# Optimization experiments

Measured on AMD Instinct MI355X. Metric: run time of the kernel, lower is better.

## Reference

```python
import jax, jax.numpy as jnp
import numpy as np

D = 1024      # d_model
H = 16        # num_heads
DK = D // H   # head dim
L = 6         # num_layers
DFF = 4 * D   # feed-forward width
V = 32000     # vocab
B = 8         # batch
TP1 = 513     # target tokens (x length); decoded length = 512
S = 1024      # encoder frames
MAXLEN = 512
EPS = 1e-6


def make_pe(max_len, d):
    pos = np.arange(max_len, dtype=np.float64)[:, None]
    i = np.arange(0, d, 2, dtype=np.float64)[None, :]
    ang = pos / np.power(10000.0, i / d)
    pe = np.zeros((max_len, d), dtype=np.float32)
    pe[:, 0::2] = np.sin(ang)
    pe[:, 1::2] = np.cos(ang)
    return jnp.asarray(pe)


def setup_inputs() -> dict:
    key = jax.random.key(0)
    ks = jax.random.split(key, 16)
    sc = 0.02
    inp = {
        'x': jax.random.randint(ks[0], (B, TP1), 0, V, dtype=jnp.int64),
        'encoder_output': jax.random.normal(ks[1], (B, S, D), jnp.float32),
        'emb': jax.random.normal(ks[2], (V, D), jnp.float32) * sc,
        'pe': make_pe(MAXLEN, D),
        # per-layer stacked params; index 0..3 = q,k,v,out projections (in,out layout)
        'attn1_w': jax.random.normal(ks[3], (L, 4, D, D), jnp.float32) * sc,
        'attn1_b': jnp.zeros((L, 4, D), jnp.float32),
        'attn2_w': jax.random.normal(ks[4], (L, 4, D, D), jnp.float32) * sc,
        'attn2_b': jnp.zeros((L, 4, D), jnp.float32),
        'norm_a': jnp.ones((L, 3, D), jnp.float32),
        'norm_b': jnp.zeros((L, 3, D), jnp.float32),
        'ff1_w': jax.random.normal(ks[5], (L, D, DFF), jnp.float32) * sc,
        'ff1_b': jnp.zeros((L, DFF), jnp.float32),
        'ff2_w': jax.random.normal(ks[6], (L, DFF, D), jnp.float32) * sc,
        'ff2_b': jnp.zeros((L, D), jnp.float32),
        'fc_w': jax.random.normal(ks[7], (D, V), jnp.float32) * sc,
        'fc_b': jnp.zeros((V,), jnp.float32),
    }
    return inp


def _norm(x, a, b):
    mu = jnp.mean(x, axis=-1, keepdims=True)
    # torch .std() default is unbiased (ddof=1)
    var = jnp.sum((x - mu) ** 2, axis=-1, keepdims=True) / (x.shape[-1] - 1)
    return a * (x - mu) / (jnp.sqrt(var) + EPS) + b


def _mha(q_in, kv_in, w, b):
    # w: [4, D, D], b: [4, D]; masks in the original are no-ops (bug), omitted.
    bs, tq, _ = q_in.shape
    q = (q_in @ w[0] + b[0]).reshape(bs, tq, H, DK).transpose(0, 2, 1, 3)
    k = (kv_in @ w[1] + b[1]).reshape(bs, -1, H, DK).transpose(0, 2, 1, 3)
    v = (kv_in @ w[2] + b[2]).reshape(bs, -1, H, DK).transpose(0, 2, 1, 3)
    score = jnp.einsum('bhqd,bhkd->bhqk', q, k) / np.sqrt(DK).astype(np.float32)
    attn = jax.nn.softmax(score, axis=-1)
    o = jnp.einsum('bhqk,bhkd->bhqd', attn, v)
    o = o.transpose(0, 2, 1, 3).reshape(bs, tq, D)
    return o @ w[3] + b[3]


def reference(x, encoder_output, emb, pe, attn1_w, attn1_b, attn2_w, attn2_b,
              norm_a, norm_b, ff1_w, ff1_b, ff2_w, ff2_b, fc_w, fc_b):
    t = x.shape[1] - 1
    h = emb[x[:, :-1]] + pe[None, :t, :]  # [B, T, D]
    for l in range(L):
        a1 = _mha(h, h, attn1_w[l], attn1_b[l])
        h = _norm(a1 + h, norm_a[l, 0], norm_b[l, 0])
        a2 = _mha(h, encoder_output, attn2_w[l], attn2_b[l])
        h = _norm(a2 + h, norm_a[l, 1], norm_b[l, 1])
        f = jax.nn.relu(h @ ff1_w[l] + ff1_b[l]) @ ff2_w[l] + ff2_b[l]
        h = _norm(f + h, norm_a[l, 2], norm_b[l, 2])
    logits = h @ fc_w + fc_b  # [B, T, V]
    return jax.nn.log_softmax(logits, axis=-1)
```

## Files before the change

kernel.cpp:

```cpp
#include <hip/hip_runtime.h>

typedef __attribute__((ext_vector_type(4))) float f32x4;
typedef __attribute__((ext_vector_type(8))) __bf16 bfx8;
typedef unsigned short u16;
typedef unsigned int u32;

__device__ __forceinline__ u16 f2bf(float f) {
  u32 u = __builtin_bit_cast(u32, f);
  u = (u + 0x7FFFu + ((u >> 16) & 1u)) >> 16;
  return (u16)u;
}
__device__ __forceinline__ float bf2f(u16 u) {
  return __builtin_bit_cast(float, ((u32)u) << 16);
}

typedef __attribute__((address_space(1))) const void gvoid;
typedef __attribute__((address_space(3))) void svoid;
__device__ __forceinline__ void gload16(const void* g, void* l) {
  __builtin_amdgcn_global_load_lds((gvoid*)g, (svoid*)l, 16, 0, 0);
}

__device__ __forceinline__ float wredsum(float v) {
#pragma unroll
  for (int o = 32; o; o >>= 1) v += __shfl_xor(v, o, 64);
  return v;
}
__device__ __forceinline__ float wredmax(float v) {
#pragma unroll
  for (int o = 32; o; o >>= 1) v = fmaxf(v, __shfl_xor(v, o, 64));
  return v;
}

__global__ __launch_bounds__(256) void wconv_kernel(const float* __restrict__ in,
                                                    u16* __restrict__ out, int K, int N) {
  __shared__ u16 tile[32][33];
  const long z = blockIdx.z;
  const float* iz = in + z * (long)K * N;
  u16* oz = out + z * (long)K * N;
  const int n0 = blockIdx.x << 5, k0 = blockIdx.y << 5;
  const int tx = threadIdx.x & 31, ty = threadIdx.x >> 5;
#pragma unroll
  for (int i = 0; i < 4; ++i)
    tile[ty + 8 * i][tx] = f2bf(iz[(long)(k0 + ty + 8 * i) * N + n0 + tx]);
  __syncthreads();
#pragma unroll
  for (int i = 0; i < 4; ++i)
    oz[(long)(n0 + ty + 8 * i) * K + k0 + tx] = tile[tx][ty + 8 * i];
}

__global__ __launch_bounds__(256) void cvt_kernel(const float* __restrict__ in,
                                                  u16* __restrict__ out, long n) {
  long i = ((long)blockIdx.x * 256 + threadIdx.x) * 4;
  if (i + 3 < n) {
    float4 v = *(const float4*)(in + i);
    ushort4 o = {f2bf(v.x), f2bf(v.y), f2bf(v.z), f2bf(v.w)};
    *(ushort4*)(out + i) = o;
  }
}

__global__ __launch_bounds__(256) void embed_kernel(const int* __restrict__ x,
                                                    const float* __restrict__ emb,
                                                    const float* __restrict__ pe,
                                                    float* __restrict__ h,
                                                    u16* __restrict__ hb) {
  const int row = blockIdx.x;
  const int b = row >> 9, t = row & 511;
  const long tok = (long)x[b * 513 + t];
  const int d = threadIdx.x << 2;
  float4 e = *(const float4*)(emb + tok * 1024 + d);
  float4 p = *(const float4*)(pe + (long)t * 1024 + d);
  float4 v = {e.x + p.x, e.y + p.y, e.z + p.z, e.w + p.w};
  *(float4*)(h + (long)row * 1024 + d) = v;
  ushort4 o = {f2bf(v.x), f2bf(v.y), f2bf(v.z), f2bf(v.w)};
  *(ushort4*)(hb + (long)row * 1024 + d) = o;
}

__global__ __launch_bounds__(256) void addnorm_kernel(const float* __restrict__ delta,
                                                      float* __restrict__ h,
                                                      u16* __restrict__ hb,
                                                      const float* __restrict__ ga,
                                                      const float* __restrict__ gb) {
  __shared__ float r1[4], r2[4];
  const long row = blockIdx.x;
  const int d = threadIdx.x << 2;
  float4 a = *(const float4*)(h + row * 1024 + d);
  float4 q = *(const float4*)(delta + row * 1024 + d);
  float x0 = a.x + q.x, x1 = a.y + q.y, x2 = a.z + q.z, x3 = a.w + q.w;
  float s1 = wredsum(x0 + x1 + x2 + x3);
  float s2 = wredsum(x0 * x0 + x1 * x1 + x2 * x2 + x3 * x3);
  if ((threadIdx.x & 63) == 0) { r1[threadIdx.x >> 6] = s1; r2[threadIdx.x >> 6] = s2; }
  __syncthreads();
  float S1 = r1[0] + r1[1] + r1[2] + r1[3];
  float S2 = r2[0] + r2[1] + r2[2] + r2[3];
  float mu = S1 * (1.0f / 1024.0f);
  float var = (S2 - S1 * mu) * (1.0f / 1023.0f);
  float inv = 1.0f / (sqrtf(fmaxf(var, 0.f)) + 1e-6f);
  float4 g4 = *(const float4*)(ga + d);
  float4 b4 = *(const float4*)(gb + d);
  float y0 = g4.x * (x0 - mu) * inv + b4.x;
  float y1 = g4.y * (x1 - mu) * inv + b4.y;
  float y2 = g4.z * (x2 - mu) * inv + b4.z;
  float y3 = g4.w * (x3 - mu) * inv + b4.w;
  float4 y = {y0, y1, y2, y3};
  *(float4*)(h + row * 1024 + d) = y;
  ushort4 o = {f2bf(y0), f2bf(y1), f2bf(y2), f2bf(y3)};
  *(ushort4*)(hb + row * 1024 + d) = o;
}

__global__ __launch_bounds__(256) void logsoftmax_kernel(float* __restrict__ lg) {
  const long row = blockIdx.x;
  float* lr = lg + row * 32000L;
  float m = -1e30f, s = 0.f;
  for (int j = threadIdx.x; j < 8000; j += 256) {
    float4 v = *(const float4*)(lr + (long)j * 4);
    float lm = fmaxf(fmaxf(v.x, v.y), fmaxf(v.z, v.w));
    if (lm > m) { s *= __expf(m - lm); m = lm; }
    s += __expf(v.x - m) + __expf(v.y - m) + __expf(v.z - m) + __expf(v.w - m);
  }
#pragma unroll
  for (int o = 32; o; o >>= 1) {
    float om = __shfl_xor(m, o, 64), os = __shfl_xor(s, o, 64);
    float M = fmaxf(m, om);
    s = s * __expf(m - M) + os * __expf(om - M);
    m = M;
  }
  __shared__ float rm[4], rs[4];
  if ((threadIdx.x & 63) == 0) { rm[threadIdx.x >> 6] = m; rs[threadIdx.x >> 6] = s; }
  __syncthreads();
  float M = fmaxf(fmaxf(rm[0], rm[1]), fmaxf(rm[2], rm[3]));
  float S = rs[0] * __expf(rm[0] - M) + rs[1] * __expf(rm[1] - M) +
            rs[2] * __expf(rm[2] - M) + rs[3] * __expf(rm[3] - M);
  float lse = M + __logf(S);
  for (int j = threadIdx.x; j < 8000; j += 256) {
    float4 v = *(const float4*)(lr + (long)j * 4);
    v.x -= lse; v.y -= lse; v.z -= lse; v.w -= lse;
    *(float4*)(lr + (long)j * 4) = v;
  }
}

__global__ __launch_bounds__(512) void logsoftmax_bf16_kernel(const u16* __restrict__ lg,
                                                              float* __restrict__ out) {
  __shared__ float rr[8];
  const long row = blockIdx.x;
  const u16* lr = lg + row * 32000L;
  float* od = out + row * 32000L;
  const int tid = threadIdx.x;
  float m0 = -1e30f, m1 = -1e30f;
  for (int j = tid * 8; j < 32000; j += 4096) {
    ushort4 a = *(const ushort4*)(lr + j);
    ushort4 b = *(const ushort4*)(lr + j + 4);
    m0 = fmaxf(m0, fmaxf(fmaxf(bf2f(a.x), bf2f(a.y)), fmaxf(bf2f(a.z), bf2f(a.w))));
    m1 = fmaxf(m1, fmaxf(fmaxf(bf2f(b.x), bf2f(b.y)), fmaxf(bf2f(b.z), bf2f(b.w))));
  }
  float m = wredmax(fmaxf(m0, m1));
  if ((tid & 63) == 0) rr[tid >> 6] = m;
  __syncthreads();
  m = fmaxf(fmaxf(fmaxf(rr[0], rr[1]), fmaxf(rr[2], rr[3])),
            fmaxf(fmaxf(rr[4], rr[5]), fmaxf(rr[6], rr[7])));
  __syncthreads();
  float s0 = 0.f, s1 = 0.f;
  for (int j = tid * 8; j < 32000; j += 4096) {
    ushort4 a = *(const ushort4*)(lr + j);
    ushort4 b = *(const ushort4*)(lr + j + 4);
    s0 += __expf(bf2f(a.x) - m) + __expf(bf2f(a.y) - m) +
          __expf(bf2f(a.z) - m) + __expf(bf2f(a.w) - m);
    s1 += __expf(bf2f(b.x) - m) + __expf(bf2f(b.y) - m) +
          __expf(bf2f(b.z) - m) + __expf(bf2f(b.w) - m);
  }
  float s = wredsum(s0 + s1);
  if ((tid & 63) == 0) rr[tid >> 6] = s;
  __syncthreads();
  s = rr[0] + rr[1] + rr[2] + rr[3] + rr[4] + rr[5] + rr[6] + rr[7];
  const float lse = m + __logf(s);
  for (int j = tid * 8; j < 32000; j += 4096) {
    ushort4 a = *(const ushort4*)(lr + j);
    ushort4 b = *(const ushort4*)(lr + j + 4);
    float4 o0 = {bf2f(a.x) - lse, bf2f(a.y) - lse, bf2f(a.z) - lse, bf2f(a.w) - lse};
    float4 o1 = {bf2f(b.x) - lse, bf2f(b.y) - lse, bf2f(b.z) - lse, bf2f(b.w) - lse};
    *(float4*)(od + j) = o0;
    *(float4*)(od + j + 4) = o1;
  }
}

template <int SKV>
__global__ __launch_bounds__(256) void attn_kernel(const u16* __restrict__ Q,
                                                   const u16* __restrict__ Kb,
                                                   const u16* __restrict__ Vt,
                                                   u16* __restrict__ ctx) {
  __shared__ u16 Kl[4096];
  __shared__ u16 Vl[4096];
  __shared__ u16 Pl[4][16][72];
  const int tid = threadIdx.x, lane = tid & 63, wave = tid >> 6;
  const int l15 = lane & 15, lg = lane >> 4;
  const int bh = blockIdx.y;
  const int qrow = blockIdx.x * 64 + wave * 16 + l15;
  const u16* qp = Q + ((long)bh * 512 + qrow) * 64 + lg * 8;
  bfx8 qf0 = *(const bfx8*)(qp);
  bfx8 qf1 = *(const bfx8*)(qp + 32);

  const int srow = tid >> 3;
  const int schunk = (tid & 7) ^ (srow & 7);
  const u16* Kbb = Kb + ((long)bh * SKV + srow) * 64 + schunk * 8;
  const u16* Vtb2 = Vt + ((long)bh * 64 + srow) * SKV + schunk * 8;

  const f32x4 zf = {0.f, 0.f, 0.f, 0.f};
  f32x4 acc_o[4] = {zf, zf, zf, zf};
  float mrun = -1e30f, lrun = 0.f;
  const int swk = l15 & 7;

#pragma unroll 1
  for (int kv0 = 0; kv0 < SKV; kv0 += 64) {
    gload16(Kbb + (long)kv0 * 64, &Kl[tid * 8]);
    gload16(Kbb + (long)(kv0 + 32) * 64, &Kl[2048 + tid * 8]);
    gload16(Vtb2 + kv0, &Vl[tid * 8]);
    gload16(Vtb2 + (long)32 * SKV + kv0, &Vl[2048 + tid * 8]);
    __syncthreads();
    f32x4 sacc[4];
#pragma unroll
    for (int kvt = 0; kvt < 4; ++kvt) {
      const int krow = kvt * 16 + l15;
      bfx8 kf0 = *(const bfx8*)&Kl[krow * 64 + ((lg ^ swk) << 3)];
      bfx8 kf1 = *(const bfx8*)&Kl[krow * 64 + (((4 + lg) ^ swk) << 3)];
      f32x4 t = __builtin_amdgcn_mfma_f32_16x16x32_bf16(kf0, qf0, zf, 0, 0, 0);
      sacc[kvt] = __builtin_amdgcn_mfma_f32_16x16x32_bf16(kf1, qf1, t, 0, 0, 0);
    }
    float pm = -1e30f;
#pragma unroll
    for (int kvt = 0; kvt < 4; ++kvt)
#pragma unroll
      for (int r = 0; r < 4; ++r) pm = fmaxf(pm, sacc[kvt][r]);
    pm = fmaxf(pm, __shfl_xor(pm, 16, 64));
    pm = fmaxf(pm, __shfl_xor(pm, 32, 64));
    pm *= 0.125f;
    const float mnew = fmaxf(mrun, pm);
    const float corr = __expf(mrun - mnew);
    float psum = 0.f;
#pragma unroll
    for (int kvt = 0; kvt < 4; ++kvt)
#pragma unroll
      for (int r = 0; r < 4; ++r) {
        float p = __expf(sacc[kvt][r] * 0.125f - mnew);
        psum += p;
        Pl[wave][l15][kvt * 16 + lg * 4 + r] = f2bf(p);
      }
    psum += __shfl_xor(psum, 16, 64);
    psum += __shfl_xor(psum, 32, 64);
    lrun = lrun * corr + psum;
    mrun = mnew;
#pragma unroll
    for (int dt = 0; dt < 4; ++dt) {
      acc_o[dt][0] *= corr; acc_o[dt][1] *= corr;
      acc_o[dt][2] *= corr; acc_o[dt][3] *= corr;
    }
    bfx8 pf0 = *(const bfx8*)&Pl[wave][l15][lg * 8];
    bfx8 pf1 = *(const bfx8*)&Pl[wave][l15][32 + lg * 8];
#pragma unroll
    for (int dt = 0; dt < 4; ++dt) {
      const int vrow = dt * 16 + l15;
      bfx8 vf0 = *(const bfx8*)&Vl[vrow * 64 + ((lg ^ swk) << 3)];
      bfx8 vf1 = *(const bfx8*)&Vl[vrow * 64 + (((4 + lg) ^ swk) << 3)];
      acc_o[dt] = __builtin_amdgcn_mfma_f32_16x16x32_bf16(vf0, pf0, acc_o[dt], 0, 0, 0);
      acc_o[dt] = __builtin_amdgcn_mfma_f32_16x16x32_bf16(vf1, pf1, acc_o[dt], 0, 0, 0);
    }
    __syncthreads();
  }
  const float inv = 1.0f / lrun;
  const int b = bh >> 4, hh = bh & 15;
  u16* crow = ctx + ((long)b * 512 + qrow) * 1024 + hh * 64;
#pragma unroll
  for (int dt = 0; dt < 4; ++dt)
#pragma unroll
    for (int r = 0; r < 4; ++r)
      crow[dt * 16 + lg * 4 + r] = f2bf(acc_o[dt][r] * inv);
}

template <int BM, int BN, int WMW, int WNW, int EPI, bool RELU>
__global__ __launch_bounds__(256) void gemm_bt(const u16* __restrict__ A, long sAz, int lda,
                                               const u16* __restrict__ Bt, long sBz, int ldb,
                                               const float* __restrict__ bias,
                                               void* __restrict__ out, long sCz, int ldc,
                                               int K, int Ttok) {
  constexpr int WROWS = BM / WMW, WCOLS = BN / WNW;
  constexpr int MI = WROWS / 16, NI = WCOLS / 16;
  __shared__ u16 As[BM * 32];
  __shared__ u16 Bs[BN * 32];
  const int tid = threadIdx.x, lane = tid & 63, wave = tid >> 6;
  const int l15 = lane & 15, lg = lane >> 4;
  const int wm = wave / WNW, wn = wave % WNW;
  const int bx = blockIdx.x, by = blockIdx.y;
  const long z = blockIdx.z;
  const int srow = tid >> 2, scol = (tid & 3) << 3;
  const u16* Aa = A + z * sAz + (long)(by * BM + srow) * lda + scol;
  const u16* Ba = Bt + z * sBz + (long)(bx * BN + srow) * ldb + scol;

  f32x4 acc[MI][NI];
#pragma unroll
  for (int i = 0; i < MI; ++i)
#pragma unroll
    for (int j = 0; j < NI; ++j) acc[i][j] = (f32x4){0.f, 0.f, 0.f, 0.f};

  for (int kt = 0; kt < K; kt += 32) {
#pragma unroll
    for (int i = 0; i < BM / 64; ++i)
      gload16(Aa + (long)i * 64 * lda + kt, &As[i * 2048 + tid * 8]);
#pragma unroll
    for (int i = 0; i < BN / 64; ++i)
      gload16(Ba + (long)i * 64 * ldb + kt, &Bs[i * 2048 + tid * 8]);
    __syncthreads();
    bfx8 afr[MI], bfr[NI];
#pragma unroll
    for (int i = 0; i < MI; ++i)
      afr[i] = *(const bfx8*)&As[(wm * WROWS + i * 16 + l15) * 32 + (lg << 3)];
#pragma unroll
    for (int j = 0; j < NI; ++j)
      bfr[j] = *(const bfx8*)&Bs[(wn * WCOLS + j * 16 + l15) * 32 + (lg << 3)];
#pragma unroll
    for (int i = 0; i < MI; ++i)
#pragma unroll
      for (int j = 0; j < NI; ++j)
        acc[i][j] = __builtin_amdgcn_mfma_f32_16x16x32_bf16(afr[i], bfr[j], acc[i][j], 0, 0, 0);
    __syncthreads();
  }

  const int gm0 = by * BM + wm * WROWS;
  const int gn0 = bx * BN + wn * WCOLS;
#pragma unroll
  for (int i = 0; i < MI; ++i) {
#pragma unroll
    for (int j = 0; j < NI; ++j) {
      const int gn = gn0 + j * 16 + l15;
      const float bv = bias ? bias[gn] : 0.f;
#pragma unroll
      for (int r = 0; r < 4; ++r) {
        const int gm = gm0 + i * 16 + (lg << 2) + r;
        float v = acc[i][j][r] + bv;
        if (RELU) v = fmaxf(v, 0.f);
        if constexpr (EPI == 0) {
          ((float*)out)[z * sCz + (long)gm * ldc + gn] = v;
        } else if constexpr (EPI == 1) {
          ((u16*)out)[z * sCz + (long)gm * ldc + gn] = f2bf(v);
        } else if constexpr (EPI == 3) {
          const int b = gm / Ttok, t = gm - b * Ttok;
          const int hh = gn >> 6, dk = gn & 63;
          ((u16*)out)[(((long)(b * 16 + hh) * Ttok + t) << 6) + dk] = f2bf(v);
        }
      }
    }
  }
}

#define MMAQ(hm, hn)                                                                   \
  {                                                                                    \
    _Pragma("unroll") for (int kk = 0; kk < 2; ++kk)                                   \
        _Pragma("unroll") for (int i = 0; i < 4; ++i)                                  \
            _Pragma("unroll") for (int jn = 0; jn < 2; ++jn)                           \
                acc[(hm)*4 + i][(hn)*2 + jn] = __builtin_amdgcn_mfma_f32_16x16x32_bf16( \
                    a[i][kk], b[jn][kk], acc[(hm)*4 + i][(hn)*2 + jn], 0, 0, 0);       \
  }

template <int EPI, bool RELU>
__global__ __launch_bounds__(512, 2) void gemm256(const u16* __restrict__ A, int lda,
                                                  const u16* __restrict__ Bt, int ldb,
                                                  const float* __restrict__ bias,
                                                  void* __restrict__ out, int ldc, int K,
                                                  int Ttok, void* __restrict__ out2,
                                                  void* __restrict__ out3, int gx) {
  __shared__ u16 lds[2][2][2][8192];
  const int tid = threadIdx.x, lane = tid & 63;
  const int wid = tid >> 6, wm = wid >> 2, wn = wid & 3;
  const int l15 = lane & 15, lg = lane >> 4;
  const int nwg = gridDim.x;
  int wg = blockIdx.x;
  wg = (wg & 7) * (nwg >> 3) + (wg >> 3);
  const int mt = wg % gx, nt_ = wg / gx;
  const int NT = K >> 6;

  const int r0 = tid >> 3;
  const int blkx = (tid & 7) ^ (r0 & 7);
  const u16* Abase = A + (long)(mt * 256 + r0) * lda + blkx * 8;
  const u16* Bbase = Bt + (long)(nt_ * 256 + r0) * ldb + blkx * 8;

  auto stageA = [&](int s, int half) {
    const int kts = (s < NT ? s : NT - 1) << 6;
    const u16* g = Abase + (long)(half * 128) * lda + kts;
    gload16(g, &lds[s & 1][0][half][tid * 8]);
    gload16(g + (long)64 * lda, &lds[s & 1][0][half][(512 + tid) * 8]);
  };
  auto stageB = [&](int s, int half) {
    const int kts = (s < NT ? s : NT - 1) << 6;
    const u16* g = Bbase + (long)(half * 128) * ldb + kts;
    gload16(g, &lds[s & 1][1][half][tid * 8]);
    gload16(g + (long)64 * ldb, &lds[s & 1][1][half][(512 + tid) * 8]);
  };

  f32x4 acc[8][4];
#pragma unroll
  for (int i = 0; i < 8; ++i)
#pragma unroll
    for (int j = 0; j < 4; ++j) acc[i][j] = (f32x4){0.f, 0.f, 0.f, 0.f};
  bfx8 a[4][2], b[2][2];

  const int sw = l15 & 7;
  auto loadA = [&](int buf, int hm) {
#pragma unroll
    for (int i = 0; i < 4; ++i) {
      const int row = hm * 64 + i * 16 + l15;
#pragma unroll
      for (int kk = 0; kk < 2; ++kk)
        a[i][kk] = *(const bfx8*)&lds[buf][0][wm][row * 64 + (((kk * 4 + lg) ^ sw) << 3)];
    }
  };
  auto loadB = [&](int buf, int hn) {
#pragma unroll
    for (int jn = 0; jn < 2; ++jn) {
      const int row = (wn & 1) * 64 + hn * 32 + jn * 16 + l15;
#pragma unroll
      for (int kk = 0; kk < 2; ++kk)
        b[jn][kk] = *(const bfx8*)&lds[buf][1][wn >> 1][row * 64 + (((kk * 4 + lg) ^ sw) << 3)];
    }
  };

  stageA(0, 0); stageA(0, 1); stageB(0, 0); stageB(0, 1);
  stageA(1, 0); stageA(1, 1);
  asm volatile("s_waitcnt vmcnt(4)" ::: "memory");
  __builtin_amdgcn_s_barrier();

  for (int t = 0; t < NT; ++t) {
    const int p = t & 1;
    loadA(p, 0); loadB(p, 0);
    stageB(t + 1, 0);
    __builtin_amdgcn_s_barrier();
    asm volatile("s_waitcnt lgkmcnt(0)" ::: "memory");
    __builtin_amdgcn_s_setprio(1);
    MMAQ(0, 0);
    __builtin_amdgcn_s_setprio(0);
    __builtin_amdgcn_s_barrier();
    loadB(p, 1);
    stageB(t + 1, 1);
    __builtin_amdgcn_s_barrier();
    asm volatile("s_waitcnt lgkmcnt(0)" ::: "memory");
    __builtin_amdgcn_s_setprio(1);
    MMAQ(0, 1);
    __builtin_amdgcn_s_setprio(0);
    __builtin_amdgcn_s_barrier();
    loadA(p, 1); loadB(p, 0);
    stageA(t + 2, 0);
    __builtin_amdgcn_s_barrier();
    asm volatile("s_waitcnt lgkmcnt(0)" ::: "memory");
    __builtin_amdgcn_s_setprio(1);
    MMAQ(1, 0);
    __builtin_amdgcn_s_setprio(0);
    __builtin_amdgcn_s_barrier();
    loadB(p, 1);
    stageA(t + 2, 1);
    asm volatile("s_waitcnt vmcnt(4)" ::: "memory");
    __builtin_amdgcn_s_barrier();
    asm volatile("s_waitcnt lgkmcnt(0)" ::: "memory");
    __builtin_amdgcn_s_setprio(1);
    MMAQ(1, 1);
    __builtin_amdgcn_s_setprio(0);
    __builtin_amdgcn_s_barrier();
  }

  const int gm0 = mt * 256 + wm * 128;
  const int gn0 = nt_ * 256 + wn * 64;
#pragma unroll
  for (int ii = 0; ii < 8; ++ii) {
#pragma unroll
    for (int jj = 0; jj < 4; ++jj) {
      const int gn = gn0 + jj * 16 + l15;
      const float bv = bias ? bias[gn] : 0.f;
#pragma unroll
      for (int r = 0; r < 4; ++r) {
        const int gm = gm0 + ii * 16 + (lg << 2) + r;
        float v = acc[ii][jj][r] + bv;
        if (RELU) v = fmaxf(v, 0.f);
        if constexpr (EPI == 0) {
          ((float*)out)[(long)gm * ldc + gn] = v;
        } else if constexpr (EPI == 1) {
          ((u16*)out)[(long)gm * ldc + gn] = f2bf(v);
        } else if constexpr (EPI == 6) {
          const int bq = gm / Ttok, t2 = gm - bq * Ttok;
          const int sec = gn >> 10, w1 = gn & 1023;
          const int hh = w1 >> 6, dk = w1 & 63;
          const u16 val = f2bf(v);
          if (sec == 0)
            ((u16*)out)[(((long)(bq * 16 + hh) * Ttok + t2) << 6) + dk] = val;
          else if (sec == 1)
            ((u16*)out2)[(((long)(bq * 16 + hh) * Ttok + t2) << 6) + dk] = val;
          else
            ((u16*)out3)[((long)((bq * 16 + hh) << 6) + dk) * Ttok + t2] = val;
        } else if constexpr (EPI == 7) {
          const int bq = gm / Ttok, t2 = gm - bq * Ttok;
          const int sec = gn >> 10, w1 = gn & 1023;
          const int hh = w1 >> 6, dk = w1 & 63;
          const u16 val = f2bf(v);
          if (sec == 0)
            ((u16*)out)[(((long)(bq * 16 + hh) * Ttok + t2) << 6) + dk] = val;
          else
            ((u16*)out2)[((long)((bq * 16 + hh) << 6) + dk) * Ttok + t2] = val;
        }
      }
    }
  }
}

extern "C" void kernel_launch(void* const* d_in, const int* in_sizes, int n_in,
                              void* d_out, int out_size, void* d_ws, size_t ws_size,
                              hipStream_t stream) {
  const int* x = (const int*)d_in[0];
  const float* enc = (const float*)d_in[1];
  const float* emb = (const float*)d_in[2];
  const float* pe = (const float*)d_in[3];
  const float* a1w = (const float*)d_in[4];
  const float* a1b = (const float*)d_in[5];
  const float* a2w = (const float*)d_in[6];
  const float* a2b = (const float*)d_in[7];
  const float* nra = (const float*)d_in[8];
  const float* nrb = (const float*)d_in[9];
  const float* f1w = (const float*)d_in[10];
  const float* f1b = (const float*)d_in[11];
  const float* f2w = (const float*)d_in[12];
  const float* f2b = (const float*)d_in[13];
  const float* fcw = (const float*)d_in[14];
  const float* fcb = (const float*)d_in[15];
  float* out = (float*)d_out;

  char* base = (char*)d_ws;
  size_t off = 0;
  auto alloc = [&](size_t bytes) -> void* {
    void* p = base + off;
    off += (bytes + 255) & ~(size_t)255;
    return p;
  };
  const long wsz = 1024 * 1024;
  const bool big = ws_size >= (600ull << 20);
  u16* wT = (u16*)alloc(96ull * wsz * 2);
  u16* encb = (u16*)alloc(8ull * wsz * 2);
  float* h = (float*)alloc(4ull * wsz * 4);
  u16* hb = (u16*)alloc(4ull * wsz * 2);
  u16* qb = (u16*)alloc(4ull * wsz * 2);
  u16* kb = (u16*)alloc(8ull * wsz * 2);
  u16* vtb = (u16*)alloc(8ull * wsz * 2);
  u16* ctxb = (u16*)alloc(4ull * wsz * 2);
  float* af = (float*)alloc(4ull * wsz * 4);
  u16* midb = (u16*)alloc(16ull * wsz * 2);
  u16* fcT = qb;
  u16* lgb = big ? (u16*)alloc(4096ull * 32000 * 2) : nullptr;

  u16* wTa1 = wT;
  u16* wTa2 = wT + 24 * wsz;
  u16* wTf1 = wT + 48 * wsz;
  u16* wTf2 = wT + 72 * wsz;

  cvt_kernel<<<dim3(8192), dim3(256), 0, stream>>>(enc, encb, 8ll * wsz);
  embed_kernel<<<dim3(4096), dim3(256), 0, stream>>>(x, emb, pe, h, hb);
  wconv_kernel<<<dim3(32, 32, 24), dim3(256), 0, stream>>>(a1w, wTa1, 1024, 1024);
  wconv_kernel<<<dim3(32, 32, 24), dim3(256), 0, stream>>>(a2w, wTa2, 1024, 1024);
  wconv_kernel<<<dim3(128, 32, 6), dim3(256), 0, stream>>>(f1w, wTf1, 1024, 4096);
  wconv_kernel<<<dim3(32, 128, 6), dim3(256), 0, stream>>>(f2w, wTf2, 4096, 1024);

  for (int l = 0; l < 6; ++l) {
    const float* b1 = a1b + (long)l * 4096;
    const float* b2 = a2b + (long)l * 4096;
    const u16* w1 = wTa1 + (long)l * 4 * wsz;
    const u16* w2 = wTa2 + (long)l * 4 * wsz;

    gemm256<6, false><<<dim3(192), dim3(512), 0, stream>>>(
        hb, 1024, w1, 1024, b1, qb, 0, 1024, 512, kb, vtb, 16);
    attn_kernel<512><<<dim3(8, 128), dim3(256), 0, stream>>>(qb, kb, vtb, ctxb);
    gemm_bt<128, 128, 2, 2, 0, false><<<dim3(8, 32, 1), dim3(256), 0, stream>>>(
        ctxb, 0, 1024, w1 + 3 * wsz, 0, 1024, b1 + 3072, af, 0, 1024, 1024, 0);
    addnorm_kernel<<<dim3(4096), dim3(256), 0, stream>>>(af, h, hb, nra + (l * 3 + 0) * 1024,
                                                         nrb + (l * 3 + 0) * 1024);

    gemm_bt<128, 128, 2, 2, 3, false><<<dim3(8, 32, 1), dim3(256), 0, stream>>>(
        hb, 0, 1024, w2, 0, 1024, b2, qb, 0, 0, 1024, 512);
    gemm256<7, false><<<dim3(256), dim3(512), 0, stream>>>(
        encb, 1024, w2 + wsz, 1024, b2 + 1024, kb, 0, 1024, 1024, vtb, nullptr, 32);
    attn_kernel<1024><<<dim3(8, 128), dim3(256), 0, stream>>>(qb, kb, vtb, ctxb);
    gemm_bt<128, 128, 2, 2, 0, false><<<dim3(8, 32, 1), dim3(256), 0, stream>>>(
        ctxb, 0, 1024, w2 + 3 * wsz, 0, 1024, b2 + 3072, af, 0, 1024, 1024, 0);
    addnorm_kernel<<<dim3(4096), dim3(256), 0, stream>>>(af, h, hb, nra + (l * 3 + 1) * 1024,
                                                         nrb + (l * 3 + 1) * 1024);

    gemm256<1, true><<<dim3(256), dim3(512), 0, stream>>>(
        hb, 1024, wTf1 + (long)l * 4 * wsz, 1024, f1b + (long)l * 4096, midb, 4096, 1024, 0,
        nullptr, nullptr, 16);
    gemm_bt<128, 128, 2, 2, 0, false><<<dim3(8, 32, 1), dim3(256), 0, stream>>>(
        midb, 0, 4096, wTf2 + (long)l * 4 * wsz, 0, 4096, f2b + (long)l * 1024, af, 0, 1024,
        4096, 0);
    addnorm_kernel<<<dim3(4096), dim3(256), 0, stream>>>(af, h, hb, nra + (l * 3 + 2) * 1024,
                                                         nrb + (l * 3 + 2) * 1024);
  }

  wconv_kernel<<<dim3(1000, 32, 1), dim3(256), 0, stream>>>(fcw, fcT, 1024, 32000);
  if (big) {
    gemm256<1, false><<<dim3(2000), dim3(512), 0, stream>>>(
        hb, 1024, fcT, 1024, fcb, lgb, 32000, 1024, 0, nullptr, nullptr, 16);
    logsoftmax_bf16_kernel<<<dim3(4096), dim3(512), 0, stream>>>(lgb, out);
  } else {
    gemm256<0, false><<<dim3(2000), dim3(512), 0, stream>>>(
        hb, 1024, fcT, 1024, fcb, out, 32000, 1024, 0, nullptr, nullptr, 16);
    logsoftmax_kernel<<<dim3(4096), dim3(256), 0, stream>>>(out);
  }
}
```

Baseline: 3.652 ms.

## Split-K the N=1024 GEMMs, sum partials in addnorm, cache logits rows in LDS

The output-projection and FF2 GEMMs now run 2-way split-K (grid z=2). Each split writes a separate fp32 partial, bias is applied only on z=0, and addnorm sums both partials with the residual. This doubles the block count from 256 to 512 so more work is in flight, at the cost of one extra fp32 partial buffer written and read per addnorm. The bf16 log-softmax stages each 32000-element row into 64KB of LDS, so the max, sum and output passes read global logits once instead of three times, which may lower occupancy. The gemm256 block-to-tile mapping is also changed for XCD locality.

```diff
diff --git a/kernel.cpp b/kernel.cpp
--- a/kernel.cpp
+++ b/kernel.cpp
@@ -76,6 +76,7 @@
 }
 
 __global__ __launch_bounds__(256) void addnorm_kernel(const float* __restrict__ delta,
+                                                      const float* __restrict__ delta2,
                                                       float* __restrict__ h,
                                                       u16* __restrict__ hb,
                                                       const float* __restrict__ ga,
@@ -85,7 +86,9 @@
   const int d = threadIdx.x << 2;
   float4 a = *(const float4*)(h + row * 1024 + d);
   float4 q = *(const float4*)(delta + row * 1024 + d);
-  float x0 = a.x + q.x, x1 = a.y + q.y, x2 = a.z + q.z, x3 = a.w + q.w;
+  float4 q2 = *(const float4*)(delta2 + row * 1024 + d);
+  float x0 = a.x + q.x + q2.x, x1 = a.y + q.y + q2.y;
+  float x2 = a.z + q.z + q2.z, x3 = a.w + q.w + q2.w;
   float s1 = wredsum(x0 + x1 + x2 + x3);
   float s2 = wredsum(x0 * x0 + x1 * x1 + x2 * x2 + x3 * x3);
   if ((threadIdx.x & 63) == 0) { r1[threadIdx.x >> 6] = s1; r2[threadIdx.x >> 6] = s2; }
@@ -140,6 +143,7 @@
 
 __global__ __launch_bounds__(512) void logsoftmax_bf16_kernel(const u16* __restrict__ lg,
                                                               float* __restrict__ out) {
+  __shared__ u16 rl[32000];
   __shared__ float rr[8];
   const long row = blockIdx.x;
   const u16* lr = lg + row * 32000L;
@@ -149,6 +153,8 @@
   for (int j = tid * 8; j < 32000; j += 4096) {
     ushort4 a = *(const ushort4*)(lr + j);
     ushort4 b = *(const ushort4*)(lr + j + 4);
+    *(ushort4*)&rl[j] = a;
+    *(ushort4*)&rl[j + 4] = b;
     m0 = fmaxf(m0, fmaxf(fmaxf(bf2f(a.x), bf2f(a.y)), fmaxf(bf2f(a.z), bf2f(a.w))));
     m1 = fmaxf(m1, fmaxf(fmaxf(bf2f(b.x), bf2f(b.y)), fmaxf(bf2f(b.z), bf2f(b.w))));
   }
@@ -160,8 +166,8 @@
   __syncthreads();
   float s0 = 0.f, s1 = 0.f;
   for (int j = tid * 8; j < 32000; j += 4096) {
-    ushort4 a = *(const ushort4*)(lr + j);
-    ushort4 b = *(const ushort4*)(lr + j + 4);
+    ushort4 a = *(const ushort4*)&rl[j];
+    ushort4 b = *(const ushort4*)&rl[j + 4];
     s0 += __expf(bf2f(a.x) - m) + __expf(bf2f(a.y) - m) +
           __expf(bf2f(a.z) - m) + __expf(bf2f(a.w) - m);
     s1 += __expf(bf2f(b.x) - m) + __expf(bf2f(b.y) - m) +
@@ -173,8 +179,8 @@
   s = rr[0] + rr[1] + rr[2] + rr[3] + rr[4] + rr[5] + rr[6] + rr[7];
   const float lse = m + __logf(s);
   for (int j = tid * 8; j < 32000; j += 4096) {
-    ushort4 a = *(const ushort4*)(lr + j);
-    ushort4 b = *(const ushort4*)(lr + j + 4);
+    ushort4 a = *(const ushort4*)&rl[j];
+    ushort4 b = *(const ushort4*)&rl[j + 4];
     float4 o0 = {bf2f(a.x) - lse, bf2f(a.y) - lse, bf2f(a.z) - lse, bf2f(a.w) - lse};
     float4 o1 = {bf2f(b.x) - lse, bf2f(b.y) - lse, bf2f(b.z) - lse, bf2f(b.w) - lse};
     *(float4*)(od + j) = o0;
@@ -329,7 +335,7 @@
 #pragma unroll
     for (int j = 0; j < NI; ++j) {
       const int gn = gn0 + j * 16 + l15;
-      const float bv = bias ? bias[gn] : 0.f;
+      const float bv = (bias && z == 0) ? bias[gn] : 0.f;
 #pragma unroll
       for (int r = 0; r < 4; ++r) {
         const int gm = gm0 + i * 16 + (lg << 2) + r;
@@ -369,10 +375,10 @@
   const int tid = threadIdx.x, lane = tid & 63;
   const int wid = tid >> 6, wm = wid >> 2, wn = wid & 3;
   const int l15 = lane & 15, lg = lane >> 4;
-  const int nwg = gridDim.x;
-  int wg = blockIdx.x;
-  wg = (wg & 7) * (nwg >> 3) + (wg >> 3);
-  const int mt = wg % gx, nt_ = wg / gx;
+  const int S = gx >> 3;
+  const int xcd = blockIdx.x & 7, idx = blockIdx.x >> 3;
+  const int mt = xcd * S + idx % S;
+  const int nt_ = idx / S;
   const int NT = K >> 6;
 
   const int r0 = tid >> 3;
@@ -544,6 +550,7 @@
   u16* vtb = (u16*)alloc(8ull * wsz * 2);
   u16* ctxb = (u16*)alloc(4ull * wsz * 2);
   float* af = (float*)alloc(4ull * wsz * 4);
+  float* af2 = (float*)alloc(4ull * wsz * 4);
   u16* midb = (u16*)alloc(16ull * wsz * 2);
   u16* fcT = qb;
   u16* lgb = big ? (u16*)alloc(4096ull * 32000 * 2) : nullptr;
@@ -569,29 +576,29 @@
     gemm256<6, false><<<dim3(192), dim3(512), 0, stream>>>(
         hb, 1024, w1, 1024, b1, qb, 0, 1024, 512, kb, vtb, 16);
     attn_kernel<512><<<dim3(8, 128), dim3(256), 0, stream>>>(qb, kb, vtb, ctxb);
-    gemm_bt<128, 128, 2, 2, 0, false><<<dim3(8, 32, 1), dim3(256), 0, stream>>>(
-        ctxb, 0, 1024, w1 + 3 * wsz, 0, 1024, b1 + 3072, af, 0, 1024, 1024, 0);
-    addnorm_kernel<<<dim3(4096), dim3(256), 0, stream>>>(af, h, hb, nra + (l * 3 + 0) * 1024,
-                                                         nrb + (l * 3 + 0) * 1024);
+    gemm_bt<128, 128, 2, 2, 0, false><<<dim3(8, 32, 2), dim3(256), 0, stream>>>(
+        ctxb, 512, 1024, w1 + 3 * wsz, 512, 1024, b1 + 3072, af, 4194304, 1024, 512, 0);
+    addnorm_kernel<<<dim3(4096), dim3(256), 0, stream>>>(
+        af, af2, h, hb, nra + (l * 3 + 0) * 1024, nrb + (l * 3 + 0) * 1024);
 
     gemm_bt<128, 128, 2, 2, 3, false><<<dim3(8, 32, 1), dim3(256), 0, stream>>>(
         hb, 0, 1024, w2, 0, 1024, b2, qb, 0, 0, 1024, 512);
     gemm256<7, false><<<dim3(256), dim3(512), 0, stream>>>(
         encb, 1024, w2 + wsz, 1024, b2 + 1024, kb, 0, 1024, 1024, vtb, nullptr, 32);
     attn_kernel<1024><<<dim3(8, 128), dim3(256), 0, stream>>>(qb, kb, vtb, ctxb);
-    gemm_bt<128, 128, 2, 2, 0, false><<<dim3(8, 32, 1), dim3(256), 0, stream>>>(
-        ctxb, 0, 1024, w2 + 3 * wsz, 0, 1024, b2 + 3072, af, 0, 1024, 1024, 0);
-    addnorm_kernel<<<dim3(4096), dim3(256), 0, stream>>>(af, h, hb, nra + (l * 3 + 1) * 1024,
-                                                         nrb + (l * 3 + 1) * 1024);
+    gemm_bt<128, 128, 2, 2, 0, false><<<dim3(8, 32, 2), dim3(256), 0, stream>>>(
+        ctxb, 512, 1024, w2 + 3 * wsz, 512, 1024, b2 + 3072, af, 4194304, 1024, 512, 0);
+    addnorm_kernel<<<dim3(4096), dim3(256), 0, stream>>>(
+        af, af2, h, hb, nra + (l * 3 + 1) * 1024, nrb + (l * 3 + 1) * 1024);
 
     gemm256<1, true><<<dim3(256), dim3(512), 0, stream>>>(
         hb, 1024, wTf1 + (long)l * 4 * wsz, 1024, f1b + (long)l * 4096, midb, 4096, 1024, 0,
         nullptr, nullptr, 16);
-    gemm_bt<128, 128, 2, 2, 0, false><<<dim3(8, 32, 1), dim3(256), 0, stream>>>(
-        midb, 0, 4096, wTf2 + (long)l * 4 * wsz, 0, 4096, f2b + (long)l * 1024, af, 0, 1024,
-        4096, 0);
-    addnorm_kernel<<<dim3(4096), dim3(256), 0, stream>>>(af, h, hb, nra + (l * 3 + 2) * 1024,
-                                                         nrb + (l * 3 + 2) * 1024);
+    gemm_bt<128, 128, 2, 2, 0, false><<<dim3(8, 32, 2), dim3(256), 0, stream>>>(
+        midb, 2048, 4096, wTf2 + (long)l * 4 * wsz, 2048, 4096, f2b + (long)l * 1024, af,
+        4194304, 1024, 2048, 0);
+    addnorm_kernel<<<dim3(4096), dim3(256), 0, stream>>>(
+        af, af2, h, hb, nra + (l * 3 + 2) * 1024, nrb + (l * 3 + 2) * 1024);
   }
 
   wconv_kernel<<<dim3(1000, 32, 1), dim3(256), 0, stream>>>(fcw, fcT, 1024, 32000);
```

Result: faster. 3.211 ms (-12.1%).
